# Kernel tuning notes

Measured on AMD Instinct MI355X. Metric: run time of the kernel, lower is better.

The kernel has to match this reference:

```python
import jax, jax.numpy as jnp
import numpy as np

N, D, DH, H = 2048, 256, 256, 4
DHEAD = DH // H
NEG = -1e30


def setup_inputs() -> dict:
    key = jax.random.key(0)
    ks = jax.random.split(key, 24)
    s = 0.05
    inp = {
        'axiom_states': jax.random.normal(ks[0], (N, D), jnp.float32),
        'adj0': (jax.random.uniform(ks[1], (N, N)) < 0.015).astype(jnp.float32),
        'adj1': (jax.random.uniform(ks[2], (N, N)) < 0.015).astype(jnp.float32),
        'w0': jax.random.uniform(ks[3], (N, N), jnp.float32),
        'w1': jax.random.uniform(ks[4], (N, N), jnp.float32),
        'Wm0': jax.random.normal(ks[5], (DH, D), jnp.float32) * s,
        'bm0': jax.random.normal(ks[6], (DH,), jnp.float32) * s,
        'Wa0': jax.random.normal(ks[7], (H, 2 * D), jnp.float32) * s,
        'ba0': jax.random.normal(ks[8], (H,), jnp.float32) * s,
        'Wm1': jax.random.normal(ks[9], (DH, D), jnp.float32) * s,
        'bm1': jax.random.normal(ks[10], (DH,), jnp.float32) * s,
        'Wa1': jax.random.normal(ks[11], (H, 2 * D), jnp.float32) * s,
        'ba1': jax.random.normal(ks[12], (H,), jnp.float32) * s,
        'gru_wih': jax.random.normal(ks[13], (3 * D, 2 * DH), jnp.float32) * s,
        'gru_whh': jax.random.normal(ks[14], (3 * D, D), jnp.float32) * s,
        'gru_bih': jax.random.normal(ks[15], (3 * D,), jnp.float32) * s,
        'gru_bhh': jax.random.normal(ks[16], (3 * D,), jnp.float32) * s,
        'ln_g': jnp.ones((D,), jnp.float32),
        'ln_b': jnp.zeros((D,), jnp.float32),
    }
    return inp


def _edge_messages(x, adj, w, Wm, bm, Wa, ba):
    # GAT-style decomposition of Linear([x_i, x_j]) -> a_cur[i] + a_nb[j] + b
    a_cur = x @ Wa[:, :D].T                      # [N,H] (target i, first half of concat)
    a_nb = x @ Wa[:, D:].T                       # [N,H] (neighbor j, second half)
    s = a_nb[:, None, :] + a_cur[None, :, :] + ba  # [j,i,H]
    s = jax.nn.leaky_relu(s, 0.2)
    s = s * w[:, :, None]                        # edge-weight scaled scores (pre-softmax)
    mask = adj != 0                              # edge j -> i iff adj[j,i] != 0
    logits = jnp.where(mask[:, :, None], s, NEG)
    attn = jax.nn.softmax(logits, axis=0) * mask[:, :, None]  # zero for isolated nodes
    msg = (x @ Wm.T + bm).reshape(N, H, DHEAD)   # per-neighbor messages
    agg = jnp.einsum('jih,jhd->ihd', attn, msg)  # softmax-weighted sum over neighbors
    return agg.reshape(N, DH)


def _forward(axiom_states, adj0, adj1, w0, w1, Wm0, bm0, Wa0, ba0,
             Wm1, bm1, Wa1, ba1, gru_wih, gru_whh, gru_bih, gru_bhh, ln_g, ln_b):
    m0 = _edge_messages(axiom_states, adj0, w0, Wm0, bm0, Wa0, ba0)
    m1 = _edge_messages(axiom_states, adj1, w1, Wm1, bm1, Wa1, ba1)
    msg = jnp.concatenate([m0, m1], axis=-1)     # dropout is identity in eval
    # GRUCell (torch semantics)
    gi = msg @ gru_wih.T + gru_bih
    gh = axiom_states @ gru_whh.T + gru_bhh
    r = jax.nn.sigmoid(gi[:, :D] + gh[:, :D])
    z = jax.nn.sigmoid(gi[:, D:2 * D] + gh[:, D:2 * D])
    n = jnp.tanh(gi[:, 2 * D:] + r * gh[:, 2 * D:])
    h = (1.0 - z) * n + z * axiom_states
    # LayerNorm
    mu = jnp.mean(h, axis=-1, keepdims=True)
    var = jnp.var(h, axis=-1, keepdims=True)
    return (h - mu) * jax.lax.rsqrt(var + 1e-5) * ln_g + ln_b


def reference(axiom_states, adj0, adj1, w0, w1, Wm0, bm0, Wa0, ba0,
              Wm1, bm1, Wa1, ba1, gru_wih, gru_whh, gru_bih, gru_bhh, ln_g, ln_b):
    return _forward(axiom_states, adj0, adj1, w0, w1, Wm0, bm0, Wa0, ba0,
                    Wm1, bm1, Wa1, ba1, gru_wih, gru_whh, gru_bih, gru_bhh, ln_g, ln_b)
```

## Files before the change

### kernel.cpp

```cpp
#include <hip/hip_runtime.h>

#define NN 2048
#define DD 256
#define HH 4
#define PW 1280
#define ECAP 128

typedef unsigned short ushort_t;
typedef __attribute__((ext_vector_type(4))) unsigned short us4;
typedef __attribute__((ext_vector_type(8))) short s8;
typedef __attribute__((ext_vector_type(4))) float f4;

__device__ __forceinline__ ushort_t f2b(float f) {
    unsigned int u = __float_as_uint(f);
    return (ushort_t)((u + 0x7fffu + ((u >> 16) & 1u)) >> 16);
}
__device__ __forceinline__ float b2f(ushort_t b) {
    return __uint_as_float(((unsigned int)b) << 16);
}
__device__ __forceinline__ void gl_lds16(const void* g, void* l) {
    __builtin_amdgcn_global_load_lds(
        (const __attribute__((address_space(1))) void*)g,
        (__attribute__((address_space(3))) void*)l, 16, 0, 0);
}

#define E_EB  256
#define E_XC  768
#define E_WC  1088
#define E_WI  1472
#define E_NB  1600

__global__ __launch_bounds__(256) void prep_kernel(
    const float* __restrict__ x,
    const float* __restrict__ adj0, const float* __restrict__ adj1,
    const float* __restrict__ w0, const float* __restrict__ w1,
    const float* __restrict__ Wm0, const float* __restrict__ Wm1,
    const float* __restrict__ whh, const float* __restrict__ wih,
    const float* __restrict__ Wa0, const float* __restrict__ Wa1,
    int* __restrict__ cnt, uint2* __restrict__ ejw,
    ushort_t* __restrict__ xb, ushort_t* __restrict__ Wcatb, ushort_t* __restrict__ wihb,
    float* __restrict__ acur, float* __restrict__ anb)
{
    __shared__ float sh[16][257];
    const int b = blockIdx.x, t = threadIdx.x;

    if (b < E_EB) {
        const int l = b & 1, chunk = b >> 1;
        const int i0 = chunk * 16;
        const float* adj = l ? adj1 : adj0;
        const float* w   = l ? w1 : w0;
        int* lcnt = (int*)sh;
        if (t < 16) lcnt[t] = 0;
        __syncthreads();
        const int rowLane = t >> 2, q = t & 3;
        #pragma unroll 2
        for (int r0r = 0; r0r < NN; r0r += 64) {
            const int j = r0r + rowLane;
            const float4 a  = *(const float4*)(adj + (size_t)j * NN + i0 + q * 4);
            const float4 qw = *(const float4*)(w   + (size_t)j * NN + i0 + q * 4);
            const float av[4] = {a.x, a.y, a.z, a.w};
            const float qv[4] = {qw.x, qw.y, qw.z, qw.w};
            #pragma unroll
            for (int u = 0; u < 4; ++u) {
                if (av[u] != 0.f) {
                    const int li = q * 4 + u;
                    const int slot = atomicAdd(&lcnt[li], 1);
                    if (slot < ECAP) {
                        uint2 pk;
                        pk.x = (unsigned int)j;
                        pk.y = __float_as_uint(qv[u]);
                        ejw[((size_t)l * NN + i0 + li) * ECAP + slot] = pk;
                    }
                }
            }
        }
        __syncthreads();
        if (t < 16) cnt[l * NN + i0 + t] = lcnt[t];
        return;
    }
    if (b < E_XC) {
        const int id = (b - E_EB) * 1024 + t * 4;
        const float4 v = *(const float4*)(x + id);
        us4 o; o.x = f2b(v.x); o.y = f2b(v.y); o.z = f2b(v.z); o.w = f2b(v.w);
        *(us4*)(xb + id) = o;
        return;
    }
    if (b < E_WC) {
        const int id = (b - E_XC) * 1024 + t * 4;
        const int c = id >> 8, k = id & 255;
        const float* src = (c < 256) ? Wm0 + (size_t)c * DD + k
                         : (c < 512) ? Wm1 + (size_t)(c - 256) * DD + k
                                     : whh + (size_t)(c - 512) * DD + k;
        const float4 v = *(const float4*)src;
        us4 o; o.x = f2b(v.x); o.y = f2b(v.y); o.z = f2b(v.z); o.w = f2b(v.w);
        *(us4*)(Wcatb + id) = o;
        return;
    }
    if (b < E_WI) {
        const int id = (b - E_WC) * 1024 + t * 4;
        const float4 v = *(const float4*)(wih + id);
        us4 o; o.x = f2b(v.x); o.y = f2b(v.y); o.z = f2b(v.z); o.w = f2b(v.w);
        *(us4*)(wihb + id) = o;
        return;
    }
    {
        const int i0 = (b - E_WI) * 16;
        for (int rr = 0; rr < 16; ++rr)
            sh[rr][t] = x[(size_t)(i0 + rr) * DD + t];
        __syncthreads();
        const int r = t >> 4, idx = t & 15;
        const int l = idx >> 3, isnb = (idx >> 2) & 1, h = idx & 3;
        const float* wrow = (l ? Wa1 : Wa0) + h * (2 * DD) + isnb * DD;
        float acc = 0.f;
        for (int k = 0; k < DD; ++k) acc = fmaf(sh[r][k], wrow[k], acc);
        float* dst = isnb ? anb : acur;
        dst[((size_t)l * NN + i0 + r) * HH + h] = acc;
    }
}

__device__ __forceinline__ void gemm_core(
    const ushort_t* __restrict__ A, int lda, const ushort_t* __restrict__ B, int ldb,
    int r0, int c0, int K, ushort_t (*as)[64], ushort_t (*bs)[64], f4 acc[2][2])
{
    const int t = threadIdx.x;
    const int wave = t >> 6, lane = t & 63;
    const int wm = (wave & 1) * 32, wn = (wave >> 1) * 32;
    const int fm = lane & 15, fq = lane >> 4;

    const int m0q0 = wave * 16 + (lane >> 3);
    const int m0q1 = m0q0 + 8;
    const int cs0 = ((lane & 7) ^ (m0q0 & 7)) * 8;
    const int cs1 = ((lane & 7) ^ (m0q1 & 7)) * 8;
    const ushort_t* ga0 = A + (size_t)(r0 + m0q0) * lda + cs0;
    const ushort_t* ga1 = A + (size_t)(r0 + m0q1) * lda + cs1;
    const ushort_t* gb0 = B + (size_t)(c0 + m0q0) * ldb + cs0;
    const ushort_t* gb1 = B + (size_t)(c0 + m0q1) * ldb + cs1;
    ushort_t* la0 = &as[wave * 16][0];
    ushort_t* la1 = &as[wave * 16 + 8][0];
    ushort_t* lb0 = &bs[wave * 16][0];
    ushort_t* lb1 = &bs[wave * 16 + 8][0];
    const int ra0 = wm + fm, ra1 = wm + 16 + fm;
    const int rb0 = wn + fm, rb1 = wn + 16 + fm;

    for (int k0 = 0; k0 < K; k0 += 64) {
        __syncthreads();
        gl_lds16(ga0 + k0, la0);
        gl_lds16(ga1 + k0, la1);
        gl_lds16(gb0 + k0, lb0);
        gl_lds16(gb1 + k0, lb1);
        __syncthreads();
        #pragma unroll
        for (int kk = 0; kk < 2; ++kk) {
            const int cc = kk * 4 + fq;
            const s8 a0 = *(const s8*)&as[ra0][(cc ^ (ra0 & 7)) * 8];
            const s8 a1 = *(const s8*)&as[ra1][(cc ^ (ra1 & 7)) * 8];
            const s8 b0 = *(const s8*)&bs[rb0][(cc ^ (rb0 & 7)) * 8];
            const s8 b1 = *(const s8*)&bs[rb1][(cc ^ (rb1 & 7)) * 8];
            acc[0][0] = __builtin_amdgcn_mfma_f32_16x16x32_bf16(a0, b0, acc[0][0], 0, 0, 0);
            acc[0][1] = __builtin_amdgcn_mfma_f32_16x16x32_bf16(a0, b1, acc[0][1], 0, 0, 0);
            acc[1][0] = __builtin_amdgcn_mfma_f32_16x16x32_bf16(a1, b0, acc[1][0], 0, 0, 0);
            acc[1][1] = __builtin_amdgcn_mfma_f32_16x16x32_bf16(a1, b1, acc[1][1], 0, 0, 0);
        }
    }
}

__global__ __launch_bounds__(256) void gemm1_kernel(
    const ushort_t* __restrict__ xb, const ushort_t* __restrict__ Wcatb,
    const float* __restrict__ bm0, const float* __restrict__ bm1,
    const float* __restrict__ bhh,
    ushort_t* __restrict__ msgb, float* __restrict__ gh)
{
    __shared__ ushort_t as[64][64];
    __shared__ ushort_t bs[64][64];
    const int t = threadIdx.x;
    const int wave = t >> 6, lane = t & 63;
    const int wm = (wave & 1) * 32, wn = (wave >> 1) * 32;
    const int fm = lane & 15, fq = lane >> 4;
    const int c0 = blockIdx.x * 64, r0 = blockIdx.y * 64;
    f4 acc[2][2] = {};
    gemm_core(xb, DD, Wcatb, DD, r0, c0, DD, as, bs, acc);
    #pragma unroll
    for (int ni = 0; ni < 2; ++ni) {
        const int col = c0 + wn + ni * 16 + fm;
        const float bv = (col < 256) ? bm0[col]
                       : (col < 512) ? bm1[col - 256]
                                     : bhh[col - 512];
        #pragma unroll
        for (int mi = 0; mi < 2; ++mi) {
            #pragma unroll
            for (int r = 0; r < 4; ++r) {
                const int row = r0 + wm + mi * 16 + fq * 4 + r;
                const float v = acc[mi][ni][r] + bv;
                if (col < 512) msgb[(size_t)row * 512 + col] = f2b(v);
                else           gh[(size_t)row * 768 + col - 512] = v;
            }
        }
    }
}

__global__ __launch_bounds__(256) void attn_kernel(
    const int* __restrict__ cnt, const uint2* __restrict__ ejw,
    const float* __restrict__ acur, const float* __restrict__ anb,
    const float* __restrict__ ba0, const float* __restrict__ ba1,
    const ushort_t* __restrict__ msgb, ushort_t* __restrict__ mcatb)
{
    const int i = blockIdx.x, l = blockIdx.y, t = threadIdx.x;
    __shared__ float es[HH][ECAP];
    __shared__ int ejs[ECAP];
    const int ne = min(max(cnt[l * NN + i], 0), ECAP);
    const float* ba = l ? ba1 : ba0;
    const size_t ebase = ((size_t)l * NN + i) * ECAP;

    if (t < ne) {
        const uint2 pk = ejw[ebase + t];
        const int j = (int)pk.x;
        const float wv = __uint_as_float(pk.y);
        ejs[t] = j;
        const float4 av = *(const float4*)(anb + ((size_t)l * NN + j) * HH);
        const float sv[4] = {av.x, av.y, av.z, av.w};
        #pragma unroll
        for (int h = 0; h < HH; ++h) {
            float s = sv[h] + acur[((size_t)l * NN + i) * HH + h] + ba[h];
            s = (s > 0.f) ? s : 0.2f * s;
            es[h][t] = s * wv;
        }
    }
    __syncthreads();
    {
        const int h = t >> 6, lane = t & 63;
        float s0 = (lane < ne) ? es[h][lane] : -1e30f;
        float s1 = (lane + 64 < ne) ? es[h][lane + 64] : -1e30f;
        float m = fmaxf(s0, s1);
        #pragma unroll
        for (int off = 32; off; off >>= 1) m = fmaxf(m, __shfl_xor(m, off));
        const float p0 = expf(s0 - m), p1 = expf(s1 - m);
        float sum = p0 + p1;
        #pragma unroll
        for (int off = 32; off; off >>= 1) sum += __shfl_xor(sum, off);
        const float inv = (ne > 0) ? 1.f / sum : 0.f;
        es[h][lane] = p0 * inv;
        if (lane + 64 < ECAP) es[h][lane + 64] = p1 * inv;
    }
    __syncthreads();
    const int h = t >> 6;
    const int off = l * DD + t;
    float acc = 0.f;
    int e = 0;
    for (; e + 4 <= ne; e += 4) {
        const float v0 = b2f(msgb[(size_t)ejs[e + 0] * 512 + off]);
        const float v1 = b2f(msgb[(size_t)ejs[e + 1] * 512 + off]);
        const float v2 = b2f(msgb[(size_t)ejs[e + 2] * 512 + off]);
        const float v3 = b2f(msgb[(size_t)ejs[e + 3] * 512 + off]);
        acc = fmaf(es[h][e + 0], v0, acc);
        acc = fmaf(es[h][e + 1], v1, acc);
        acc = fmaf(es[h][e + 2], v2, acc);
        acc = fmaf(es[h][e + 3], v3, acc);
    }
    for (; e < ne; ++e)
        acc = fmaf(es[h][e], b2f(msgb[(size_t)ejs[e] * 512 + off]), acc);
    mcatb[(size_t)i * (2 * DD) + off] = f2b(acc);
}

__global__ __launch_bounds__(256) void gemm2_kernel(
    const ushort_t* __restrict__ mcatb, const ushort_t* __restrict__ wihb,
    const float* __restrict__ bih, float* __restrict__ gi)
{
    __shared__ ushort_t as[64][64];
    __shared__ ushort_t bs[64][64];
    const int t = threadIdx.x;
    const int wave = t >> 6, lane = t & 63;
    const int wm = (wave & 1) * 32, wn = (wave >> 1) * 32;
    const int fm = lane & 15, fq = lane >> 4;
    const int c0 = blockIdx.x * 64, r0 = blockIdx.y * 64;
    f4 acc[2][2] = {};
    gemm_core(mcatb, 512, wihb, 512, r0, c0, 512, as, bs, acc);
    #pragma unroll
    for (int ni = 0; ni < 2; ++ni) {
        const int col = c0 + wn + ni * 16 + fm;
        const float bv = bih[col];
        #pragma unroll
        for (int mi = 0; mi < 2; ++mi)
            #pragma unroll
            for (int r = 0; r < 4; ++r)
                gi[(size_t)(r0 + wm + mi * 16 + fq * 4 + r) * 768 + col] =
                    acc[mi][ni][r] + bv;
    }
}

__global__ __launch_bounds__(256) void gates_ln(
    const float* __restrict__ gi, const float* __restrict__ gh, const float* __restrict__ x,
    const float* __restrict__ lng, const float* __restrict__ lnb, float* __restrict__ out)
{
    __shared__ float rs1[4], rs2[4];
    const int t = threadIdx.x;
    const int r0 = blockIdx.x * 4;
    const float gv = lng[t], bv = lnb[t];
    float hv[4];
    #pragma unroll
    for (int r = 0; r < 4; ++r) {
        const int row = r0 + r;
        const float gir = gi[(size_t)row * 768 + t];
        const float giz = gi[(size_t)row * 768 + 256 + t];
        const float gin = gi[(size_t)row * 768 + 512 + t];
        const float ghr = gh[(size_t)row * 768 + t];
        const float ghz = gh[(size_t)row * 768 + 256 + t];
        const float ghn = gh[(size_t)row * 768 + 512 + t];
        const float rr = 1.f / (1.f + expf(-(gir + ghr)));
        const float zz = 1.f / (1.f + expf(-(giz + ghz)));
        const float nn = tanhf(gin + rr * ghn);
        hv[r] = (1.f - zz) * nn + zz * x[(size_t)row * DD + t];
    }
    const int lane = t & 63, wid = t >> 6;
    for (int r = 0; r < 4; ++r) {
        float s1 = hv[r], s2 = hv[r] * hv[r];
        #pragma unroll
        for (int off = 32; off; off >>= 1) {
            s1 += __shfl_down(s1, off);
            s2 += __shfl_down(s2, off);
        }
        if (lane == 0) { rs1[wid] = s1; rs2[wid] = s2; }
        __syncthreads();
        const float sum = rs1[0] + rs1[1] + rs1[2] + rs1[3];
        const float sq  = rs2[0] + rs2[1] + rs2[2] + rs2[3];
        const float mu  = sum * (1.f / DD);
        const float var = sq * (1.f / DD) - mu * mu;
        const float inv = rsqrtf(var + 1e-5f);
        out[(size_t)(r0 + r) * DD + t] = (hv[r] - mu) * inv * gv + bv;
        __syncthreads();
    }
}

extern "C" void kernel_launch(void* const* d_in, const int* in_sizes, int n_in,
                              void* d_out, int out_size, void* d_ws, size_t ws_size,
                              hipStream_t stream)
{
    const float* x    = (const float*)d_in[0];
    const float* adj0 = (const float*)d_in[1];
    const float* adj1 = (const float*)d_in[2];
    const float* w0   = (const float*)d_in[3];
    const float* w1   = (const float*)d_in[4];
    const float* Wm0  = (const float*)d_in[5];
    const float* bm0  = (const float*)d_in[6];
    const float* Wa0  = (const float*)d_in[7];
    const float* ba0  = (const float*)d_in[8];
    const float* Wm1  = (const float*)d_in[9];
    const float* bm1  = (const float*)d_in[10];
    const float* Wa1  = (const float*)d_in[11];
    const float* ba1  = (const float*)d_in[12];
    const float* wih  = (const float*)d_in[13];
    const float* whh  = (const float*)d_in[14];
    const float* bih  = (const float*)d_in[15];
    const float* bhh  = (const float*)d_in[16];
    const float* lng  = (const float*)d_in[17];
    const float* lnb  = (const float*)d_in[18];
    float* out = (float*)d_out;

    float* ws = (float*)d_ws;
    float* gh   = ws;            ws += (size_t)NN * 768;
    float* gi   = ws;            ws += (size_t)NN * 768;
    float* acur = ws;            ws += 2 * NN * HH;
    float* anb  = ws;            ws += 2 * NN * HH;
    int*   cnt  = (int*)ws;      ws += 2 * NN;
    uint2* ejw  = (uint2*)ws;    ws += 2 * 2 * NN * ECAP;
    ushort_t* xb    = (ushort_t*)ws;  ws += (size_t)NN * DD / 2;
    ushort_t* Wcatb = (ushort_t*)ws;  ws += (size_t)PW * DD / 2;
    ushort_t* wihb  = (ushort_t*)ws;  ws += (size_t)768 * 512 / 2;
    ushort_t* msgb  = (ushort_t*)ws;  ws += (size_t)NN * 512 / 2;
    ushort_t* mcatb = (ushort_t*)ws;  ws += (size_t)NN * 512 / 2;

    prep_kernel<<<E_NB, 256, 0, stream>>>(
        x, adj0, adj1, w0, w1, Wm0, Wm1, whh, wih, Wa0, Wa1,
        cnt, ejw, xb, Wcatb, wihb, acur, anb);
    gemm1_kernel<<<dim3(PW / 64, NN / 64), 256, 0, stream>>>(
        xb, Wcatb, bm0, bm1, bhh, msgb, gh);
    attn_kernel<<<dim3(NN, 2), 256, 0, stream>>>(
        cnt, ejw, acur, anb, ba0, ba1, msgb, mcatb);
    gemm2_kernel<<<dim3(12, 32), 256, 0, stream>>>(mcatb, wihb, bih, gi);
    gates_ln<<<NN / 4, 256, 0, stream>>>(gi, gh, x, lng, lnb, out);
}
```

Before: 189.6 us.

## Split adjacency edge extraction across row groups for more prep parallelism

```diff
diff --git a/kernel.cpp b/kernel.cpp
--- a/kernel.cpp
+++ b/kernel.cpp
@@ -5,6 +5,8 @@
 #define HH 4
 #define PW 1280
 #define ECAP 128
+#define SCAP 32
+#define NG 8
 
 typedef unsigned short ushort_t;
 typedef __attribute__((ext_vector_type(4))) unsigned short us4;
@@ -24,11 +26,11 @@
         (__attribute__((address_space(3))) void*)l, 16, 0, 0);
 }
 
-#define E_EB  256
-#define E_XC  768
-#define E_WC  1088
-#define E_WI  1472
-#define E_NB  1600
+#define E_EB  2048
+#define E_XC  2560
+#define E_WC  2880
+#define E_WI  3264
+#define E_NB  3392
 
 __global__ __launch_bounds__(256) void prep_kernel(
     const float* __restrict__ x,
@@ -37,7 +39,7 @@
     const float* __restrict__ Wm0, const float* __restrict__ Wm1,
     const float* __restrict__ whh, const float* __restrict__ wih,
     const float* __restrict__ Wa0, const float* __restrict__ Wa1,
-    int* __restrict__ cnt, uint2* __restrict__ ejw,
+    int* __restrict__ cntg, uint2* __restrict__ ejw,
     ushort_t* __restrict__ xb, ushort_t* __restrict__ Wcatb, ushort_t* __restrict__ wihb,
     float* __restrict__ acur, float* __restrict__ anb)
 {
@@ -45,37 +47,43 @@
     const int b = blockIdx.x, t = threadIdx.x;
 
     if (b < E_EB) {
-        const int l = b & 1, chunk = b >> 1;
-        const int i0 = chunk * 16;
+        const int c = b & 127, l = (b >> 7) & 1, g = b >> 8;
+        const int i0 = c * 16, j0 = g * 256;
         const float* adj = l ? adj1 : adj0;
         const float* w   = l ? w1 : w0;
         int* lcnt = (int*)sh;
         if (t < 16) lcnt[t] = 0;
         __syncthreads();
         const int rowLane = t >> 2, q = t & 3;
-        #pragma unroll 2
-        for (int r0r = 0; r0r < NN; r0r += 64) {
-            const int j = r0r + rowLane;
-            const float4 a  = *(const float4*)(adj + (size_t)j * NN + i0 + q * 4);
-            const float4 qw = *(const float4*)(w   + (size_t)j * NN + i0 + q * 4);
-            const float av[4] = {a.x, a.y, a.z, a.w};
-            const float qv[4] = {qw.x, qw.y, qw.z, qw.w};
+        float4 a[4], qw[4];
+        #pragma unroll
+        for (int it = 0; it < 4; ++it) {
+            const int j = j0 + it * 64 + rowLane;
+            a[it]  = *(const float4*)(adj + (size_t)j * NN + i0 + q * 4);
+            qw[it] = *(const float4*)(w   + (size_t)j * NN + i0 + q * 4);
+        }
+        #pragma unroll
+        for (int it = 0; it < 4; ++it) {
+            const int j = j0 + it * 64 + rowLane;
+            const float av[4] = {a[it].x, a[it].y, a[it].z, a[it].w};
+            const float qv[4] = {qw[it].x, qw[it].y, qw[it].z, qw[it].w};
             #pragma unroll
             for (int u = 0; u < 4; ++u) {
                 if (av[u] != 0.f) {
                     const int li = q * 4 + u;
                     const int slot = atomicAdd(&lcnt[li], 1);
-                    if (slot < ECAP) {
+                    if (slot < SCAP) {
                         uint2 pk;
                         pk.x = (unsigned int)j;
                         pk.y = __float_as_uint(qv[u]);
-                        ejw[((size_t)l * NN + i0 + li) * ECAP + slot] = pk;
+                        ejw[(((size_t)l * NN + i0 + li) * NG + g) * SCAP + slot] = pk;
                     }
                 }
             }
         }
         __syncthreads();
-        if (t < 16) cnt[l * NN + i0 + t] = lcnt[t];
+        if (t < 16)
+            cntg[((size_t)l * NN + i0 + t) * NG + g] = min(lcnt[t], SCAP);
         return;
     }
     if (b < E_XC) {
@@ -199,7 +207,7 @@
 }
 
 __global__ __launch_bounds__(256) void attn_kernel(
-    const int* __restrict__ cnt, const uint2* __restrict__ ejw,
+    const int* __restrict__ cntg, const uint2* __restrict__ ejw,
     const float* __restrict__ acur, const float* __restrict__ anb,
     const float* __restrict__ ba0, const float* __restrict__ ba1,
     const ushort_t* __restrict__ msgb, ushort_t* __restrict__ mcatb)
@@ -207,24 +215,36 @@
     const int i = blockIdx.x, l = blockIdx.y, t = threadIdx.x;
     __shared__ float es[HH][ECAP];
     __shared__ int ejs[ECAP];
-    const int ne = min(max(cnt[l * NN + i], 0), ECAP);
+    __shared__ int scnt[NG];
     const float* ba = l ? ba1 : ba0;
-    const size_t ebase = ((size_t)l * NN + i) * ECAP;
-
-    if (t < ne) {
-        const uint2 pk = ejw[ebase + t];
-        const int j = (int)pk.x;
-        const float wv = __uint_as_float(pk.y);
-        ejs[t] = j;
-        const float4 av = *(const float4*)(anb + ((size_t)l * NN + j) * HH);
-        const float sv[4] = {av.x, av.y, av.z, av.w};
-        #pragma unroll
-        for (int h = 0; h < HH; ++h) {
-            float s = sv[h] + acur[((size_t)l * NN + i) * HH + h] + ba[h];
-            s = (s > 0.f) ? s : 0.2f * s;
-            es[h][t] = s * wv;
-        }
-    }
+    if (t < NG)
+        scnt[t] = min(max(cntg[((size_t)l * NN + i) * NG + t], 0), SCAP);
+    __syncthreads();
+    float ac[HH];
+    #pragma unroll
+    for (int h = 0; h < HH; ++h) ac[h] = acur[((size_t)l * NN + i) * HH + h] + ba[h];
+    int ne = 0;
+    #pragma unroll
+    for (int g = 0; g < NG; ++g) {
+        const int cg = scnt[g];
+        const int e = ne + t;
+        if (t < cg && e < ECAP) {
+            const uint2 pk = ejw[(((size_t)l * NN + i) * NG + g) * SCAP + t];
+            const int j = (int)pk.x;
+            const float wv = __uint_as_float(pk.y);
+            ejs[e] = j;
+            const float4 av = *(const float4*)(anb + ((size_t)l * NN + j) * HH);
+            const float sv[4] = {av.x, av.y, av.z, av.w};
+            #pragma unroll
+            for (int h = 0; h < HH; ++h) {
+                float s = sv[h] + ac[h];
+                s = (s > 0.f) ? s : 0.2f * s;
+                es[h][e] = s * wv;
+            }
+        }
+        ne += cg;
+    }
+    ne = min(ne, ECAP);
     __syncthreads();
     {
         const int h = t >> 6, lane = t & 63;
@@ -360,8 +380,8 @@
     float* gi   = ws;            ws += (size_t)NN * 768;
     float* acur = ws;            ws += 2 * NN * HH;
     float* anb  = ws;            ws += 2 * NN * HH;
-    int*   cnt  = (int*)ws;      ws += 2 * NN;
-    uint2* ejw  = (uint2*)ws;    ws += 2 * 2 * NN * ECAP;
+    int*   cntg = (int*)ws;      ws += 2 * NN * NG;
+    uint2* ejw  = (uint2*)ws;    ws += 2 * 2 * NN * NG * SCAP;
     ushort_t* xb    = (ushort_t*)ws;  ws += (size_t)NN * DD / 2;
     ushort_t* Wcatb = (ushort_t*)ws;  ws += (size_t)PW * DD / 2;
     ushort_t* wihb  = (ushort_t*)ws;  ws += (size_t)768 * 512 / 2;
@@ -370,11 +390,11 @@
 
     prep_kernel<<<E_NB, 256, 0, stream>>>(
         x, adj0, adj1, w0, w1, Wm0, Wm1, whh, wih, Wa0, Wa1,
-        cnt, ejw, xb, Wcatb, wihb, acur, anb);
+        cntg, ejw, xb, Wcatb, wihb, acur, anb);
     gemm1_kernel<<<dim3(PW / 64, NN / 64), 256, 0, stream>>>(
         xb, Wcatb, bm0, bm1, bhh, msgb, gh);
     attn_kernel<<<dim3(NN, 2), 256, 0, stream>>>(
-        cnt, ejw, acur, anb, ba0, ba1, msgb, mcatb);
+        cntg, ejw, acur, anb, ba0, ba1, msgb, mcatb);
     gemm2_kernel<<<dim3(12, 32), 256, 0, stream>>>(mcatb, wihb, bih, gi);
     gates_ln<<<NN / 4, 256, 0, stream>>>(gi, gh, x, lng, lnb, out);
 }
```

New measurement: 205.7 us. 8.5% more time.

## Move edge-list scan into GEMM1 launch and gather weights sparsely in attention

Applied to the files above, without the earlier changes.

```diff
diff --git a/kernel.cpp b/kernel.cpp
--- a/kernel.cpp
+++ b/kernel.cpp
@@ -24,69 +24,31 @@
         (__attribute__((address_space(3))) void*)l, 16, 0, 0);
 }
 
-#define E_EB  256
-#define E_XC  768
-#define E_WC  1088
-#define E_WI  1472
-#define E_NB  1600
+#define P_XC  512
+#define P_WC  832
+#define P_WI  1216
+#define P_NB  1344
 
 __global__ __launch_bounds__(256) void prep_kernel(
     const float* __restrict__ x,
-    const float* __restrict__ adj0, const float* __restrict__ adj1,
-    const float* __restrict__ w0, const float* __restrict__ w1,
     const float* __restrict__ Wm0, const float* __restrict__ Wm1,
     const float* __restrict__ whh, const float* __restrict__ wih,
     const float* __restrict__ Wa0, const float* __restrict__ Wa1,
-    int* __restrict__ cnt, uint2* __restrict__ ejw,
     ushort_t* __restrict__ xb, ushort_t* __restrict__ Wcatb, ushort_t* __restrict__ wihb,
     float* __restrict__ acur, float* __restrict__ anb)
 {
     __shared__ float sh[16][257];
     const int b = blockIdx.x, t = threadIdx.x;
 
-    if (b < E_EB) {
-        const int l = b & 1, chunk = b >> 1;
-        const int i0 = chunk * 16;
-        const float* adj = l ? adj1 : adj0;
-        const float* w   = l ? w1 : w0;
-        int* lcnt = (int*)sh;
-        if (t < 16) lcnt[t] = 0;
-        __syncthreads();
-        const int rowLane = t >> 2, q = t & 3;
-        #pragma unroll 2
-        for (int r0r = 0; r0r < NN; r0r += 64) {
-            const int j = r0r + rowLane;
-            const float4 a  = *(const float4*)(adj + (size_t)j * NN + i0 + q * 4);
-            const float4 qw = *(const float4*)(w   + (size_t)j * NN + i0 + q * 4);
-            const float av[4] = {a.x, a.y, a.z, a.w};
-            const float qv[4] = {qw.x, qw.y, qw.z, qw.w};
-            #pragma unroll
-            for (int u = 0; u < 4; ++u) {
-                if (av[u] != 0.f) {
-                    const int li = q * 4 + u;
-                    const int slot = atomicAdd(&lcnt[li], 1);
-                    if (slot < ECAP) {
-                        uint2 pk;
-                        pk.x = (unsigned int)j;
-                        pk.y = __float_as_uint(qv[u]);
-                        ejw[((size_t)l * NN + i0 + li) * ECAP + slot] = pk;
-                    }
-                }
-            }
-        }
-        __syncthreads();
-        if (t < 16) cnt[l * NN + i0 + t] = lcnt[t];
-        return;
-    }
-    if (b < E_XC) {
-        const int id = (b - E_EB) * 1024 + t * 4;
+    if (b < P_XC) {
+        const int id = b * 1024 + t * 4;
         const float4 v = *(const float4*)(x + id);
         us4 o; o.x = f2b(v.x); o.y = f2b(v.y); o.z = f2b(v.z); o.w = f2b(v.w);
         *(us4*)(xb + id) = o;
         return;
     }
-    if (b < E_WC) {
-        const int id = (b - E_XC) * 1024 + t * 4;
+    if (b < P_WC) {
+        const int id = (b - P_XC) * 1024 + t * 4;
         const int c = id >> 8, k = id & 255;
         const float* src = (c < 256) ? Wm0 + (size_t)c * DD + k
                          : (c < 512) ? Wm1 + (size_t)(c - 256) * DD + k
@@ -96,15 +58,15 @@
         *(us4*)(Wcatb + id) = o;
         return;
     }
-    if (b < E_WI) {
-        const int id = (b - E_WC) * 1024 + t * 4;
+    if (b < P_WI) {
+        const int id = (b - P_WC) * 1024 + t * 4;
         const float4 v = *(const float4*)(wih + id);
         us4 o; o.x = f2b(v.x); o.y = f2b(v.y); o.z = f2b(v.z); o.w = f2b(v.w);
         *(us4*)(wihb + id) = o;
         return;
     }
     {
-        const int i0 = (b - E_WI) * 16;
+        const int i0 = (b - P_WI) * 16;
         for (int rr = 0; rr < 16; ++rr)
             sh[rr][t] = x[(size_t)(i0 + rr) * DD + t];
         __syncthreads();
@@ -164,42 +126,83 @@
     }
 }
 
-__global__ __launch_bounds__(256) void gemm1_kernel(
+__global__ __launch_bounds__(256) void gemm1_edge_kernel(
     const ushort_t* __restrict__ xb, const ushort_t* __restrict__ Wcatb,
     const float* __restrict__ bm0, const float* __restrict__ bm1,
     const float* __restrict__ bhh,
-    ushort_t* __restrict__ msgb, float* __restrict__ gh)
+    ushort_t* __restrict__ msgb, float* __restrict__ gh,
+    const float* __restrict__ adj0, const float* __restrict__ adj1,
+    int* __restrict__ cnt, int* __restrict__ ej)
 {
     __shared__ ushort_t as[64][64];
     __shared__ ushort_t bs[64][64];
-    const int t = threadIdx.x;
-    const int wave = t >> 6, lane = t & 63;
-    const int wm = (wave & 1) * 32, wn = (wave >> 1) * 32;
-    const int fm = lane & 15, fq = lane >> 4;
-    const int c0 = blockIdx.x * 64, r0 = blockIdx.y * 64;
-    f4 acc[2][2] = {};
-    gemm_core(xb, DD, Wcatb, DD, r0, c0, DD, as, bs, acc);
-    #pragma unroll
-    for (int ni = 0; ni < 2; ++ni) {
-        const int col = c0 + wn + ni * 16 + fm;
-        const float bv = (col < 256) ? bm0[col]
-                       : (col < 512) ? bm1[col - 256]
-                                     : bhh[col - 512];
-        #pragma unroll
-        for (int mi = 0; mi < 2; ++mi) {
+    const int b = blockIdx.x, t = threadIdx.x;
+
+    if (b < 640) {
+        const int wave = t >> 6, lane = t & 63;
+        const int wm = (wave & 1) * 32, wn = (wave >> 1) * 32;
+        const int fm = lane & 15, fq = lane >> 4;
+        const int c0 = (b % 20) * 64, r0 = (b / 20) * 64;
+        f4 acc[2][2] = {};
+        gemm_core(xb, DD, Wcatb, DD, r0, c0, DD, as, bs, acc);
+        #pragma unroll
+        for (int ni = 0; ni < 2; ++ni) {
+            const int col = c0 + wn + ni * 16 + fm;
+            const float bv = (col < 256) ? bm0[col]
+                           : (col < 512) ? bm1[col - 256]
+                                         : bhh[col - 512];
             #pragma unroll
-            for (int r = 0; r < 4; ++r) {
-                const int row = r0 + wm + mi * 16 + fq * 4 + r;
-                const float v = acc[mi][ni][r] + bv;
-                if (col < 512) msgb[(size_t)row * 512 + col] = f2b(v);
-                else           gh[(size_t)row * 768 + col - 512] = v;
+            for (int mi = 0; mi < 2; ++mi) {
+                #pragma unroll
+                for (int r = 0; r < 4; ++r) {
+                    const int row = r0 + wm + mi * 16 + fq * 4 + r;
+                    const float v = acc[mi][ni][r] + bv;
+                    if (col < 512) msgb[(size_t)row * 512 + col] = f2b(v);
+                    else           gh[(size_t)row * 768 + col - 512] = v;
+                }
             }
         }
+        return;
+    }
+    {
+        const int eb = b - 640;
+        const int l = eb & 1, chunk = eb >> 1;
+        const int i0 = chunk * 16;
+        const float* adj = l ? adj1 : adj0;
+        int* lcnt = (int*)as;
+        if (t < 16) lcnt[t] = 0;
+        __syncthreads();
+        const int rowLane = t >> 2, q = t & 3;
+        for (int r0r = 0; r0r < NN; r0r += 512) {
+            float4 a[8];
+            #pragma unroll
+            for (int it = 0; it < 8; ++it) {
+                const int j = r0r + it * 64 + rowLane;
+                a[it] = *(const float4*)(adj + (size_t)j * NN + i0 + q * 4);
+            }
+            #pragma unroll
+            for (int it = 0; it < 8; ++it) {
+                const int j = r0r + it * 64 + rowLane;
+                const float av[4] = {a[it].x, a[it].y, a[it].z, a[it].w};
+                #pragma unroll
+                for (int u = 0; u < 4; ++u) {
+                    if (av[u] != 0.f) {
+                        const int li = q * 4 + u;
+                        const int slot = atomicAdd(&lcnt[li], 1);
+                        if (slot < ECAP)
+                            ej[((size_t)l * NN + i0 + li) * ECAP + slot] = j;
+                    }
+                }
+            }
+        }
+        __syncthreads();
+        if (t < 16) cnt[l * NN + i0 + t] = min(lcnt[t], ECAP);
     }
 }
 
 __global__ __launch_bounds__(256) void attn_kernel(
-    const int* __restrict__ cnt, const uint2* __restrict__ ejw,
+    const int* __restrict__ cnt, const int* __restrict__ ej,
+    const float* __restrict__ w0, const float* __restrict__ w1,
     const float* __restrict__ acur, const float* __restrict__ anb,
     const float* __restrict__ ba0, const float* __restrict__ ba1,
     const ushort_t* __restrict__ msgb, ushort_t* __restrict__ mcatb)
@@ -209,12 +212,12 @@
     __shared__ int ejs[ECAP];
     const int ne = min(max(cnt[l * NN + i], 0), ECAP);
     const float* ba = l ? ba1 : ba0;
+    const float* w  = l ? w1 : w0;
     const size_t ebase = ((size_t)l * NN + i) * ECAP;
 
     if (t < ne) {
-        const uint2 pk = ejw[ebase + t];
-        const int j = (int)pk.x;
-        const float wv = __uint_as_float(pk.y);
+        const int j = ej[ebase + t];
+        const float wv = w[(size_t)j * NN + i];
         ejs[t] = j;
         const float4 av = *(const float4*)(anb + ((size_t)l * NN + j) * HH);
         const float sv[4] = {av.x, av.y, av.z, av.w};
@@ -361,20 +364,19 @@
     float* acur = ws;            ws += 2 * NN * HH;
     float* anb  = ws;            ws += 2 * NN * HH;
     int*   cnt  = (int*)ws;      ws += 2 * NN;
-    uint2* ejw  = (uint2*)ws;    ws += 2 * 2 * NN * ECAP;
+    int*   ej   = (int*)ws;      ws += 2 * NN * ECAP;
     ushort_t* xb    = (ushort_t*)ws;  ws += (size_t)NN * DD / 2;
     ushort_t* Wcatb = (ushort_t*)ws;  ws += (size_t)PW * DD / 2;
     ushort_t* wihb  = (ushort_t*)ws;  ws += (size_t)768 * 512 / 2;
     ushort_t* msgb  = (ushort_t*)ws;  ws += (size_t)NN * 512 / 2;
     ushort_t* mcatb = (ushort_t*)ws;  ws += (size_t)NN * 512 / 2;
 
-    prep_kernel<<<E_NB, 256, 0, stream>>>(
-        x, adj0, adj1, w0, w1, Wm0, Wm1, whh, wih, Wa0, Wa1,
-        cnt, ejw, xb, Wcatb, wihb, acur, anb);
-    gemm1_kernel<<<dim3(PW / 64, NN / 64), 256, 0, stream>>>(
-        xb, Wcatb, bm0, bm1, bhh, msgb, gh);
+    prep_kernel<<<P_NB, 256, 0, stream>>>(
+        x, Wm0, Wm1, whh, wih, Wa0, Wa1, xb, Wcatb, wihb, acur, anb);
+    gemm1_edge_kernel<<<896, 256, 0, stream>>>(
+        xb, Wcatb, bm0, bm1, bhh, msgb, gh, adj0, adj1, cnt, ej);
     attn_kernel<<<dim3(NN, 2), 256, 0, stream>>>(
-        cnt, ejw, acur, anb, ba0, ba1, msgb, mcatb);
+        cnt, ej, w0, w1, acur, anb, ba0, ba1, msgb, mcatb);
     gemm2_kernel<<<dim3(12, 32), 256, 0, stream>>>(mcatb, wihb, bih, gi);
     gates_ln<<<NN / 4, 256, 0, stream>>>(gi, gh, x, lng, lnb, out);
 }
```

New measurement: 176.4 us. -6.9%, faster.
